# Kernel optimization log

Measured on AMD Instinct MI355X. Metric: run time of the kernel, lower is better.

## Reference

```python
import jax, jax.numpy as jnp
from jax import lax
import numpy as np

IMPOSSIBLE = -100000.0
B, S, T = 64, 2048, 128


def setup_inputs() -> dict:
    key = jax.random.key(0)
    k1, k2, k3, k4, k5, k6, k7 = jax.random.split(key, 7)
    emissions = jax.random.normal(k1, (B, S, T), dtype=jnp.float32)
    lengths = jax.random.randint(k2, (B,), S // 2, S + 1)  # ragged valid lengths
    mask = jnp.arange(S)[None, :] < lengths[:, None]       # (B,S) bool, contiguous
    tags = jax.random.randint(k3, (B, S), 0, T)
    forbidden_transitions = jax.random.bernoulli(k4, 0.3, (T, T))
    transitions = 0.1 * jax.random.normal(k5, (T, T), dtype=jnp.float32)
    start_transitions = 0.1 * jax.random.normal(k6, (T,), dtype=jnp.float32)
    end_transitions = 0.1 * jax.random.normal(k7, (T,), dtype=jnp.float32)
    return {
        'emissions': emissions,
        'mask': mask,
        'tags': tags,
        'forbidden_transitions': forbidden_transitions,
        'transitions': transitions,
        'start_transitions': start_transitions,
        'end_transitions': end_transitions,
    }


def _crf_nll(emissions, mask, tags, forbidden_transitions, transitions,
             start_transitions, end_transitions):
    # start/end forbidden default to all-False in the torch module, so only
    # pairwise transitions get masked.
    trans = jnp.where(forbidden_transitions, IMPOSSIBLE, transitions)  # (T,T)
    em = jnp.swapaxes(emissions, 0, 1)  # (S,B,T)
    m = mask.T                          # (S,B)
    tg = tags.T                         # (S,B)

    # ---- partition function z (logsumexp semiring forward scan) ----
    alpha0 = start_transitions[None, :] + em[0]  # (B,T)

    def fstep(alpha, xs):
        em_k, m_k = xs
        # res[b,j] = logsumexp_i( alpha[b,i] + trans[i,j] )
        res = jax.nn.logsumexp(alpha[:, :, None] + trans[None, :, :], axis=1)
        return jnp.where(m_k[:, None], res + em_k, alpha), None

    alphaF, _ = lax.scan(jax.checkpoint(fstep), alpha0, (em[1:], m[1:]))
    z = jax.nn.logsumexp(alphaF + end_transitions[None, :], axis=-1)  # (B,)

    # ---- posterior potential of the given tag sequence ----
    s0 = start_transitions[tg[0]] + jnp.take_along_axis(em[0], tg[0][:, None], axis=1)[:, 0]

    def pstep(s, xs):
        em_k, m_k, t_prev, t_k = xs
        sc = s + trans[t_prev, t_k] + jnp.take_along_axis(em_k, t_k[:, None], axis=1)[:, 0]
        return jnp.where(m_k, sc, s), None

    sF, _ = lax.scan(pstep, s0, (em[1:], m[1:], tg[:-1], tg[1:]))
    last_tag = jnp.take_along_axis(tags, (mask.sum(1) - 1)[:, None], axis=1)[:, 0]
    post = end_transitions[last_tag] + sF  # (B,)

    # torch shapes: posterior (1,B), z (1,B,1) -> broadcast (1,B,B); then mean.
    nll = post[None, None, :] - z[None, :, None]
    return jnp.mean(nll)


def reference(emissions, mask, tags, forbidden_transitions, transitions,
              start_transitions, end_transitions):
    return _crf_nll(emissions, mask, tags, forbidden_transitions, transitions,
                    start_transitions, end_transitions)
```

## Files before the change

kernel.cpp:

```cpp
#include <hip/hip_runtime.h>
#include <hip/hip_bf16.h>
#include <stdint.h>

#define BB 64
#define SS 2048
#define TT 128
#define GRP 6

typedef __bf16 bf16x8 __attribute__((ext_vector_type(8)));
typedef float  f32x4  __attribute__((ext_vector_type(4)));

__device__ __forceinline__ void wg_barrier_lds() {
    asm volatile("" ::: "memory");
    __builtin_amdgcn_s_waitcnt(0xc07f);
    __builtin_amdgcn_s_barrier();
    asm volatile("" ::: "memory");
}

__device__ __forceinline__ int detect_mode(const void* maskp) {
    uint32_t w0 = ((const uint32_t*)maskp)[0];
    if (w0 == 1u) return 0;
    if (w0 == 0x3F800000u) return 2;
    if (w0 == 0x3F803F80u) return 3;
    return 1;
}
__device__ __forceinline__ int mask_at(const void* maskp, int mode, size_t idx) {
    if (mode == 0) return ((const int*)maskp)[idx] != 0;
    if (mode == 1) return ((const unsigned char*)maskp)[idx] != 0;
    if (mode == 2) return ((const float*)maskp)[idx] != 0.f;
    return ((const unsigned short*)maskp)[idx] != 0;
}

__global__ __launch_bounds__(256, 1) void scan_kernel(
    const float* __restrict__ em, const void* __restrict__ maskp,
    const int* __restrict__ tags, const void* __restrict__ forb,
    const float* __restrict__ trans,
    const float* __restrict__ startt, const float* __restrict__ endt,
    double* __restrict__ CdW, float* __restrict__ pendW,
    float* __restrict__ uMW, double* __restrict__ postout)
{
    const int t = threadIdx.x;
    const int w = t >> 6;
    const int lane = t & 63;
    const int q = lane >> 4;
    const int c = lane & 15;
    const int bid = blockIdx.x;
    const bool isF = (bid < BB);
    const int b = isF ? bid : bid - BB;

    __shared__ __bf16 uS[2][TT];
    __shared__ __align__(16) float wred[4];
    __shared__ int    redi[4];
    __shared__ double redd[4];
    __shared__ int    redc[4];
    __shared__ float  Minit;

    const int mode = detect_mode(maskp);

    {
        int cnt = 0;
        for (int s = t; s < SS; s += 256) cnt += mask_at(maskp, mode, (size_t)b * SS + s);
        #pragma unroll
        for (int off = 32; off >= 1; off >>= 1) cnt += __shfl_xor(cnt, off);
        if (lane == 0) redi[w] = cnt;
    }
    __syncthreads();
    const int len = redi[0] + redi[1] + redi[2] + redi[3];

    const int mS    = len >> 1;
    const int steps = isF ? mS
                          : (len - 1 - mS);

    bf16x8 afrag[2][4];
    #pragma unroll
    for (int ml = 0; ml < 2; ++ml) {
        #pragma unroll
        for (int kt = 0; kt < 4; ++kt) {
            #pragma unroll
            for (int jj = 0; jj < 8; ++jj) {
                int row = isF ? (32 * kt + 8 * q + jj) : (32 * w + 16 * ml + c);
                int col = isF ? (32 * w + 16 * ml + c) : (32 * kt + 8 * q + jj);
                size_t idx = (size_t)row * TT + col;
                afrag[ml][kt][jj] = mask_at(forb, mode, idx) ? (__bf16)0.f
                                                             : (__bf16)__expf(trans[idx]);
            }
        }
    }

    const float* emB = em + (size_t)b * SS * TT;

    if (t < 16) {
        const float* base = isF ? startt : endt;
        const float* emI  = emB + (isF ? 0 : (size_t)(len - 1) * TT);
        float a[8]; float mx = -1e30f;
        #pragma unroll
        for (int jj = 0; jj < 8; ++jj) {
            int j = t * 8 + jj;
            a[jj] = base[j] + emI[j];
            mx = fmaxf(mx, a[jj]);
        }
        mx = fmaxf(mx, __shfl_xor(mx, 1)); mx = fmaxf(mx, __shfl_xor(mx, 2));
        mx = fmaxf(mx, __shfl_xor(mx, 4)); mx = fmaxf(mx, __shfl_xor(mx, 8));
        union { __bf16 h[8]; uint4 v; } pk;
        #pragma unroll
        for (int jj = 0; jj < 8; ++jj) pk.h[jj] = (__bf16)__expf(a[jj] - mx);
        *(uint4*)&uS[0][t * 8] = pk.v;
        if (t == 0) Minit = mx;
    }
    __syncthreads();

    double Cd = (double)Minit;
    float pending = 1.0f;

    const int tag0 = 32 * w + 4 * q;
    const int tag1 = tag0 + 16;

    int cur = 0;

    auto stepfn = [&](float4 e0, float4 e1, bool ren, bool scaleEm) {
        const __bf16* ub = &uS[cur][0];
        bf16x8 bf0 = *(const bf16x8*)(ub + 8 * q);
        bf16x8 bf1 = *(const bf16x8*)(ub + 32 + 8 * q);
        bf16x8 bf2 = *(const bf16x8*)(ub + 64 + 8 * q);
        bf16x8 bf3 = *(const bf16x8*)(ub + 96 + 8 * q);

        float sc00 = (scaleEm ? __expf(e0.x) : 1.0f) * pending;
        float sc01 = (scaleEm ? __expf(e0.y) : 1.0f) * pending;
        float sc02 = (scaleEm ? __expf(e0.z) : 1.0f) * pending;
        float sc03 = (scaleEm ? __expf(e0.w) : 1.0f) * pending;
        float sc10 = (scaleEm ? __expf(e1.x) : 1.0f) * pending;
        float sc11 = (scaleEm ? __expf(e1.y) : 1.0f) * pending;
        float sc12 = (scaleEm ? __expf(e1.z) : 1.0f) * pending;
        float sc13 = (scaleEm ? __expf(e1.w) : 1.0f) * pending;

        f32x4 aA0 = {0,0,0,0}, aB0 = {0,0,0,0}, aA1 = {0,0,0,0}, aB1 = {0,0,0,0};
        aA0 = __builtin_amdgcn_mfma_f32_16x16x32_bf16(afrag[0][0], bf0, aA0, 0, 0, 0);
        aA1 = __builtin_amdgcn_mfma_f32_16x16x32_bf16(afrag[1][0], bf0, aA1, 0, 0, 0);
        aB0 = __builtin_amdgcn_mfma_f32_16x16x32_bf16(afrag[0][2], bf2, aB0, 0, 0, 0);
        aB1 = __builtin_amdgcn_mfma_f32_16x16x32_bf16(afrag[1][2], bf2, aB1, 0, 0, 0);
        aA0 = __builtin_amdgcn_mfma_f32_16x16x32_bf16(afrag[0][1], bf1, aA0, 0, 0, 0);
        aA1 = __builtin_amdgcn_mfma_f32_16x16x32_bf16(afrag[1][1], bf1, aA1, 0, 0, 0);
        aB0 = __builtin_amdgcn_mfma_f32_16x16x32_bf16(afrag[0][3], bf3, aB0, 0, 0, 0);
        aB1 = __builtin_amdgcn_mfma_f32_16x16x32_bf16(afrag[1][3], bf3, aB1, 0, 0, 0);

        float v00 = (aA0[0] + aB0[0]) * sc00, v01 = (aA0[1] + aB0[1]) * sc01;
        float v02 = (aA0[2] + aB0[2]) * sc02, v03 = (aA0[3] + aB0[3]) * sc03;
        float v10 = (aA1[0] + aB1[0]) * sc10, v11 = (aA1[1] + aB1[1]) * sc11;
        float v12 = (aA1[2] + aB1[2]) * sc12, v13 = (aA1[3] + aB1[3]) * sc13;

        if (c == 0) {
            union { __bf16 h[4]; uint2 v; } p0, p1;
            p0.h[0] = (__bf16)v00; p0.h[1] = (__bf16)v01;
            p0.h[2] = (__bf16)v02; p0.h[3] = (__bf16)v03;
            p1.h[0] = (__bf16)v10; p1.h[1] = (__bf16)v11;
            p1.h[2] = (__bf16)v12; p1.h[3] = (__bf16)v13;
            __bf16* un = &uS[cur ^ 1][0];
            *(uint2*)(un + tag0) = p0.v;
            *(uint2*)(un + tag1) = p1.v;
        }
        if (ren) {
            float m = fmaxf(fmaxf(fmaxf(v00, v01), fmaxf(v02, v03)),
                            fmaxf(fmaxf(v10, v11), fmaxf(v12, v13)));
            m = fmaxf(m, __shfl_xor(m, 16));
            m = fmaxf(m, __shfl_xor(m, 32));
            if (lane == 0) wred[w] = m;
        }
        wg_barrier_lds();
        if (ren) {
            float4 wm = *(const float4*)wred;
            float M = fmaxf(fmaxf(wm.x, wm.y), fmaxf(wm.z, wm.w));
            pending = 1.0f / M;
            Cd += (double)__logf(M);
        } else {
            pending = 1.0f;
        }
        cur ^= 1;
    };

    int k = 0;
    float4 emc0[GRP], emc1[GRP];
    #pragma unroll
    for (int g = 0; g < GRP; ++g) {
        int kk = isF ? (1 + g) : (len - 2 - g);
        emc0[g] = *(const float4*)(emB + (size_t)kk * TT + tag0);
        emc1[g] = *(const float4*)(emB + (size_t)kk * TT + tag1);
    }

    while (k + GRP <= steps) {
        float4 emn0[GRP], emn1[GRP];
        #pragma unroll
        for (int g = 0; g < GRP; ++g) {
            int kk = isF ? (1 + k + GRP + g) : (len - 2 - (k + GRP + g));
            emn0[g] = *(const float4*)(emB + (size_t)kk * TT + tag0);
            emn1[g] = *(const float4*)(emB + (size_t)kk * TT + tag1);
        }
        #pragma unroll
        for (int g = 0; g < GRP; ++g)
            stepfn(emc0[g], emc1[g], g == GRP - 1, isF || (k + g != steps - 1));
        #pragma unroll
        for (int g = 0; g < GRP; ++g) { emc0[g] = emn0[g]; emc1[g] = emn1[g]; }
        k += GRP;
    }

    while (k < steps) {
        int kk = isF ? (1 + k) : (len - 2 - k);
        float4 e0 = *(const float4*)(emB + (size_t)kk * TT + tag0);
        float4 e1 = *(const float4*)(emB + (size_t)kk * TT + tag1);
        stepfn(e0, e1, true, isF || (k != steps - 1));
        ++k;
    }

    if (t < TT) uMW[(size_t)(isF ? 0 : BB) * TT + (size_t)b * TT + t] = (float)uS[cur][t];
    if (t == 0) { CdW[(isF ? 0 : BB) + b] = Cd; pendW[(isF ? 0 : BB) + b] = pending; }

    if (isF) {
        const int* tg = tags + (size_t)b * SS;
        double local = 0.0; int fcnt = 0;
        for (int kk = 1 + t; kk < len; kk += 256) {
            int tp = tg[kk - 1], tc = tg[kk];
            if (mask_at(forb, mode, (size_t)tp * TT + tc)) fcnt++;
            else local += (double)trans[tp * TT + tc];
            local += (double)emB[(size_t)kk * TT + tc];
        }
        if (t == 0) {
            local += (double)startt[tg[0]] + (double)emB[tg[0]];
            local += (double)endt[tg[len - 1]];
        }
        #pragma unroll
        for (int off = 32; off >= 1; off >>= 1) {
            local += __shfl_xor(local, off);
            fcnt  += __shfl_xor(fcnt, off);
        }
        if (lane == 0) { redd[w] = local; redc[w] = fcnt; }
        __syncthreads();
        if (t == 0) {
            double tot = redd[0] + redd[1] + redd[2] + redd[3];
            int fc = redc[0] + redc[1] + redc[2] + redc[3];
            postout[b] = tot - 100000.0 * (double)fc;
        }
    }
}

__global__ __launch_bounds__(1024) void fin_kernel(
    const double* __restrict__ CdW, const float* __restrict__ pendW,
    const float* __restrict__ uMW, const double* __restrict__ post,
    float* __restrict__ out)
{
    __shared__ double zS[BB];
    const int t = threadIdx.x, wv = t >> 6, lane = t & 63;
    for (int b = wv; b < BB; b += 16) {
        const float* uF = uMW + (size_t)b * TT;
        const float* uB = uMW + (size_t)(BB + b) * TT;
        float s = uF[lane] * uB[lane] + uF[lane + 64] * uB[lane + 64];
        #pragma unroll
        for (int off = 32; off >= 1; off >>= 1) s += __shfl_xor(s, off);
        if (lane == 0)
            zS[b] = CdW[b] + CdW[BB + b]
                  + log((double)pendW[b] * (double)pendW[BB + b] * (double)s);
    }
    __syncthreads();
    if (t < 64) {
        double pv = post[t];
        double zv = zS[t];
        #pragma unroll
        for (int off = 32; off >= 1; off >>= 1) {
            pv += __shfl_xor(pv, off);
            zv += __shfl_xor(zv, off);
        }
        if (t == 0) out[0] = (float)((pv - zv) / (double)BB);
    }
}

extern "C" void kernel_launch(void* const* d_in, const int* in_sizes, int n_in,
                              void* d_out, int out_size, void* d_ws, size_t ws_size,
                              hipStream_t stream) {
    const float* em     = (const float*)d_in[0];
    const void*  maskp  = d_in[1];
    const int*   tags   = (const int*)d_in[2];
    const void*  forb   = d_in[3];
    const float* trans  = (const float*)d_in[4];
    const float* startt = (const float*)d_in[5];
    const float* endt   = (const float*)d_in[6];

    double* post  = (double*)d_ws;
    double* CdW   = post + BB;
    float*  pendW = (float*)(CdW + 2 * BB);
    float*  uMW   = pendW + 2 * BB;

    scan_kernel<<<2 * BB, 256, 0, stream>>>(em, maskp, tags, forb, trans, startt, endt,
                                            CdW, pendW, uMW, post);
    fin_kernel<<<1, 1024, 0, stream>>>(CdW, pendW, uMW, post, (float*)d_out);
}
```

Measured before the change: 496.2 us.

## Split CRF forward scan into four segments using matrix-product middle chunks

Each sequence's scan is now cut into four parts instead of two. Forward and backward vector scans handle the ends, and two extra blocks per sequence compute full 128x128 transfer-matrix products over the middle segments, with swizzled LDS tiles. A new combine kernel applies the middle matrices to the end vectors and computes z in double precision. The serial dependency chain per block gets shorter at the price of about eight times more MFMA work per step in the middle blocks, twice as many workgroups at 512 threads, an extra kernel launch, and added bf16 rounding through the matrix products.

```diff
diff --git a/kernel.cpp b/kernel.cpp
--- a/kernel.cpp
+++ b/kernel.cpp
@@ -9,6 +9,8 @@
 
 typedef __bf16 bf16x8 __attribute__((ext_vector_type(8)));
 typedef float  f32x4  __attribute__((ext_vector_type(4)));
+
+#define SWZ(n) (((n) & 15) << 3)
 
 __device__ __forceinline__ void wg_barrier_lds() {
     asm volatile("" ::: "memory");
@@ -31,13 +33,27 @@
     return ((const unsigned short*)maskp)[idx] != 0;
 }
 
-__global__ __launch_bounds__(256, 1) void scan_kernel(
+struct EndSh {
+    __bf16 uS[2][TT];
+    float  wred[4];
+    int    redi[8];
+    double redd[8];
+    int    redc[8];
+    float  Minit;
+};
+struct MidSh {
+    __bf16 T[2][128][128];
+};
+union ShU { EndSh e; MidSh m; };
+
+__global__ __launch_bounds__(512) void scan_kernel(
     const float* __restrict__ em, const void* __restrict__ maskp,
     const int* __restrict__ tags, const void* __restrict__ forb,
     const float* __restrict__ trans,
     const float* __restrict__ startt, const float* __restrict__ endt,
     double* __restrict__ CdW, float* __restrict__ pendW,
-    float* __restrict__ uMW, double* __restrict__ postout)
+    float* __restrict__ uMW, double* __restrict__ lsW,
+    unsigned short* __restrict__ Tws, double* __restrict__ postout)
 {
     const int t = threadIdx.x;
     const int w = t >> 6;
@@ -45,230 +61,389 @@
     const int q = lane >> 4;
     const int c = lane & 15;
     const int bid = blockIdx.x;
+
+    __shared__ __align__(16) ShU sh;
+
+    const int mode = detect_mode(maskp);
+
+    const bool isEnd = (bid < 2 * BB);
     const bool isF = (bid < BB);
-    const int b = isF ? bid : bid - BB;
-
-    __shared__ __bf16 uS[2][TT];
-    __shared__ __align__(16) float wred[4];
-    __shared__ int    redi[4];
-    __shared__ double redd[4];
-    __shared__ int    redc[4];
-    __shared__ float  Minit;
-
-    const int mode = detect_mode(maskp);
+    const int seg = isEnd ? 0 : (bid - 2 * BB);
+    const int b = isEnd ? (isF ? bid : bid - BB) : (seg >> 1);
+    const int half = seg & 1;
 
     {
         int cnt = 0;
-        for (int s = t; s < SS; s += 256) cnt += mask_at(maskp, mode, (size_t)b * SS + s);
+        for (int s = t; s < SS; s += 512) cnt += mask_at(maskp, mode, (size_t)b * SS + s);
         #pragma unroll
         for (int off = 32; off >= 1; off >>= 1) cnt += __shfl_xor(cnt, off);
-        if (lane == 0) redi[w] = cnt;
+        if (lane == 0) sh.e.redi[w] = cnt;
     }
     __syncthreads();
-    const int len = redi[0] + redi[1] + redi[2] + redi[3];
-
-    const int mS    = len >> 1;
-    const int steps = isF ? mS
-                          : (len - 1 - mS);
-
-    bf16x8 afrag[2][4];
+    int len = 0;
     #pragma unroll
-    for (int ml = 0; ml < 2; ++ml) {
+    for (int i = 0; i < 8; ++i) len += sh.e.redi[i];
+    __syncthreads();
+
+    const int M  = ((len - 1) * 10) / 47;
+    const int E1 = ((len - 1) - 2 * M + 1) >> 1;
+    const int q1 = E1;
+    const int q2 = q1 + M;
+    const int q3 = q2 + M;
+    const int E2 = (len - 1) - q3;
+
+    const float* emB = em + (size_t)b * SS * TT;
+
+    if (isEnd) {
+        const int w4 = w & 3;
+        const int steps = isF ? q1 : E2;
+
+        bf16x8 afrag[2][4];
         #pragma unroll
-        for (int kt = 0; kt < 4; ++kt) {
+        for (int ml = 0; ml < 2; ++ml) {
+            #pragma unroll
+            for (int kt = 0; kt < 4; ++kt) {
+                #pragma unroll
+                for (int jj = 0; jj < 8; ++jj) {
+                    int row = isF ? (32 * kt + 8 * q + jj) : (32 * w4 + 16 * ml + c);
+                    int col = isF ? (32 * w4 + 16 * ml + c) : (32 * kt + 8 * q + jj);
+                    size_t idx = (size_t)row * TT + col;
+                    afrag[ml][kt][jj] = mask_at(forb, mode, idx) ? (__bf16)0.f
+                                                                 : (__bf16)__expf(trans[idx]);
+                }
+            }
+        }
+
+        if (t < 16) {
+            const float* base = isF ? startt : endt;
+            const float* emI  = emB + (isF ? 0 : (size_t)(len - 1) * TT);
+            float a[8]; float mx = -1e30f;
             #pragma unroll
             for (int jj = 0; jj < 8; ++jj) {
-                int row = isF ? (32 * kt + 8 * q + jj) : (32 * w + 16 * ml + c);
-                int col = isF ? (32 * w + 16 * ml + c) : (32 * kt + 8 * q + jj);
-                size_t idx = (size_t)row * TT + col;
-                afrag[ml][kt][jj] = mask_at(forb, mode, idx) ? (__bf16)0.f
-                                                             : (__bf16)__expf(trans[idx]);
-            }
-        }
-    }
-
-    const float* emB = em + (size_t)b * SS * TT;
-
-    if (t < 16) {
-        const float* base = isF ? startt : endt;
-        const float* emI  = emB + (isF ? 0 : (size_t)(len - 1) * TT);
-        float a[8]; float mx = -1e30f;
+                int j = t * 8 + jj;
+                a[jj] = base[j] + emI[j];
+                mx = fmaxf(mx, a[jj]);
+            }
+            mx = fmaxf(mx, __shfl_xor(mx, 1)); mx = fmaxf(mx, __shfl_xor(mx, 2));
+            mx = fmaxf(mx, __shfl_xor(mx, 4)); mx = fmaxf(mx, __shfl_xor(mx, 8));
+            union { __bf16 h[8]; uint4 v; } pk;
+            #pragma unroll
+            for (int jj = 0; jj < 8; ++jj) pk.h[jj] = (__bf16)__expf(a[jj] - mx);
+            *(uint4*)&sh.e.uS[0][t * 8] = pk.v;
+            if (t == 0) sh.e.Minit = mx;
+        }
+        __syncthreads();
+
+        double Cd = (double)sh.e.Minit;
+        float pending = 1.0f;
+        const int tag0 = 32 * w4 + 4 * q;
+        const int tag1 = tag0 + 16;
+        int cur = 0;
+
+        auto stepfn = [&](float4 e0, float4 e1, bool ren, bool scaleEm) {
+            const __bf16* ub = &sh.e.uS[cur][0];
+            bf16x8 bf0 = *(const bf16x8*)(ub + 8 * q);
+            bf16x8 bf1 = *(const bf16x8*)(ub + 32 + 8 * q);
+            bf16x8 bf2 = *(const bf16x8*)(ub + 64 + 8 * q);
+            bf16x8 bf3 = *(const bf16x8*)(ub + 96 + 8 * q);
+
+            float sc00 = (scaleEm ? __expf(e0.x) : 1.0f) * pending;
+            float sc01 = (scaleEm ? __expf(e0.y) : 1.0f) * pending;
+            float sc02 = (scaleEm ? __expf(e0.z) : 1.0f) * pending;
+            float sc03 = (scaleEm ? __expf(e0.w) : 1.0f) * pending;
+            float sc10 = (scaleEm ? __expf(e1.x) : 1.0f) * pending;
+            float sc11 = (scaleEm ? __expf(e1.y) : 1.0f) * pending;
+            float sc12 = (scaleEm ? __expf(e1.z) : 1.0f) * pending;
+            float sc13 = (scaleEm ? __expf(e1.w) : 1.0f) * pending;
+
+            f32x4 aA0 = {0,0,0,0}, aB0 = {0,0,0,0}, aA1 = {0,0,0,0}, aB1 = {0,0,0,0};
+            aA0 = __builtin_amdgcn_mfma_f32_16x16x32_bf16(afrag[0][0], bf0, aA0, 0, 0, 0);
+            aA1 = __builtin_amdgcn_mfma_f32_16x16x32_bf16(afrag[1][0], bf0, aA1, 0, 0, 0);
+            aB0 = __builtin_amdgcn_mfma_f32_16x16x32_bf16(afrag[0][2], bf2, aB0, 0, 0, 0);
+            aB1 = __builtin_amdgcn_mfma_f32_16x16x32_bf16(afrag[1][2], bf2, aB1, 0, 0, 0);
+            aA0 = __builtin_amdgcn_mfma_f32_16x16x32_bf16(afrag[0][1], bf1, aA0, 0, 0, 0);
+            aA1 = __builtin_amdgcn_mfma_f32_16x16x32_bf16(afrag[1][1], bf1, aA1, 0, 0, 0);
+            aB0 = __builtin_amdgcn_mfma_f32_16x16x32_bf16(afrag[0][3], bf3, aB0, 0, 0, 0);
+            aB1 = __builtin_amdgcn_mfma_f32_16x16x32_bf16(afrag[1][3], bf3, aB1, 0, 0, 0);
+
+            float v00 = (aA0[0] + aB0[0]) * sc00, v01 = (aA0[1] + aB0[1]) * sc01;
+            float v02 = (aA0[2] + aB0[2]) * sc02, v03 = (aA0[3] + aB0[3]) * sc03;
+            float v10 = (aA1[0] + aB1[0]) * sc10, v11 = (aA1[1] + aB1[1]) * sc11;
+            float v12 = (aA1[2] + aB1[2]) * sc12, v13 = (aA1[3] + aB1[3]) * sc13;
+
+            if (c == 0) {
+                union { __bf16 h[4]; uint2 v; } p0, p1;
+                p0.h[0] = (__bf16)v00; p0.h[1] = (__bf16)v01;
+                p0.h[2] = (__bf16)v02; p0.h[3] = (__bf16)v03;
+                p1.h[0] = (__bf16)v10; p1.h[1] = (__bf16)v11;
+                p1.h[2] = (__bf16)v12; p1.h[3] = (__bf16)v13;
+                __bf16* un = &sh.e.uS[cur ^ 1][0];
+                *(uint2*)(un + tag0) = p0.v;
+                *(uint2*)(un + tag1) = p1.v;
+            }
+            if (ren) {
+                float m = fmaxf(fmaxf(fmaxf(v00, v01), fmaxf(v02, v03)),
+                                fmaxf(fmaxf(v10, v11), fmaxf(v12, v13)));
+                m = fmaxf(m, __shfl_xor(m, 16));
+                m = fmaxf(m, __shfl_xor(m, 32));
+                if (lane == 0) sh.e.wred[w4] = m;
+            }
+            wg_barrier_lds();
+            if (ren) {
+                float4 wm = *(const float4*)sh.e.wred;
+                float Mx = fmaxf(fmaxf(wm.x, wm.y), fmaxf(wm.z, wm.w));
+                pending = 1.0f / Mx;
+                Cd += (double)__logf(Mx);
+            } else {
+                pending = 1.0f;
+            }
+            cur ^= 1;
+        };
+
+        int k = 0;
+        float4 emc0[GRP], emc1[GRP];
         #pragma unroll
-        for (int jj = 0; jj < 8; ++jj) {
-            int j = t * 8 + jj;
-            a[jj] = base[j] + emI[j];
-            mx = fmaxf(mx, a[jj]);
-        }
-        mx = fmaxf(mx, __shfl_xor(mx, 1)); mx = fmaxf(mx, __shfl_xor(mx, 2));
-        mx = fmaxf(mx, __shfl_xor(mx, 4)); mx = fmaxf(mx, __shfl_xor(mx, 8));
-        union { __bf16 h[8]; uint4 v; } pk;
+        for (int gg = 0; gg < GRP; ++gg) {
+            int g = isF ? gg : (GRP - 1 - gg);
+            int kk = isF ? (1 + g) : (len - 2 - g);
+            kk = kk < SS ? kk : SS - 1;
+            emc0[g] = *(const float4*)(emB + (size_t)kk * TT + tag0);
+            emc1[g] = *(const float4*)(emB + (size_t)kk * TT + tag1);
+        }
+
+        while (k + GRP <= steps) {
+            float4 emn0[GRP], emn1[GRP];
+            #pragma unroll
+            for (int gg = 0; gg < GRP; ++gg) {
+                int g = isF ? gg : (GRP - 1 - gg);
+                int kk = isF ? (1 + k + GRP + g) : (len - 2 - (k + GRP + g));
+                kk = kk < SS ? kk : SS - 1;
+                emn0[g] = *(const float4*)(emB + (size_t)kk * TT + tag0);
+                emn1[g] = *(const float4*)(emB + (size_t)kk * TT + tag1);
+            }
+            #pragma unroll
+            for (int g = 0; g < GRP; ++g)
+                stepfn(emc0[g], emc1[g], g == GRP - 1, isF || (k + g != steps - 1));
+            #pragma unroll
+            for (int g = 0; g < GRP; ++g) { emc0[g] = emn0[g]; emc1[g] = emn1[g]; }
+            k += GRP;
+        }
+        while (k < steps) {
+            int kk = isF ? (1 + k) : (len - 2 - k);
+            float4 e0 = *(const float4*)(emB + (size_t)kk * TT + tag0);
+            float4 e1 = *(const float4*)(emB + (size_t)kk * TT + tag1);
+            stepfn(e0, e1, true, isF || (k != steps - 1));
+            ++k;
+        }
+
+        __syncthreads();
+        if (t < TT) uMW[(size_t)(isF ? 0 : BB) * TT + (size_t)b * TT + t] = (float)sh.e.uS[cur][t];
+        if (t == 0) { CdW[(isF ? 0 : BB) + b] = Cd; pendW[(isF ? 0 : BB) + b] = pending; }
+
+        if (isF) {
+            const int* tg = tags + (size_t)b * SS;
+            double local = 0.0; int fcnt = 0;
+            for (int kk = 1 + t; kk < len; kk += 512) {
+                int tp = tg[kk - 1], tc = tg[kk];
+                if (mask_at(forb, mode, (size_t)tp * TT + tc)) fcnt++;
+                else local += (double)trans[tp * TT + tc];
+                local += (double)emB[(size_t)kk * TT + tc];
+            }
+            if (t == 0) {
+                local += (double)startt[tg[0]] + (double)emB[tg[0]];
+                local += (double)endt[tg[len - 1]];
+            }
+            #pragma unroll
+            for (int off = 32; off >= 1; off >>= 1) {
+                local += __shfl_xor(local, off);
+                fcnt  += __shfl_xor(fcnt, off);
+            }
+            if (lane == 0) { sh.e.redd[w] = local; sh.e.redc[w] = fcnt; }
+            __syncthreads();
+            if (t == 0) {
+                double tot = 0.0; int fc = 0;
+                #pragma unroll
+                for (int i = 0; i < 8; ++i) { tot += sh.e.redd[i]; fc += sh.e.redc[i]; }
+                postout[b] = tot - 100000.0 * (double)fc;
+            }
+        }
+    } else {
+        const int nc  = 16 * w + c;
+        const int swz = SWZ(nc);
+        const int ks  = half ? q2 : q1;
+        const int steps = M;
+
+        bf16x8 af[8][4];
         #pragma unroll
-        for (int jj = 0; jj < 8; ++jj) pk.h[jj] = (__bf16)__expf(a[jj] - mx);
-        *(uint4*)&uS[0][t * 8] = pk.v;
-        if (t == 0) Minit = mx;
+        for (int mt = 0; mt < 8; ++mt) {
+            #pragma unroll
+            for (int kt = 0; kt < 4; ++kt) {
+                #pragma unroll
+                for (int jj = 0; jj < 8; ++jj) {
+                    size_t idx = (size_t)(32 * kt + 8 * q + jj) * TT + (16 * mt + c);
+                    af[mt][kt][jj] = mask_at(forb, mode, idx) ? (__bf16)0.f
+                                                              : (__bf16)__expf(trans[idx]);
+                }
+            }
+        }
+
+        for (int p = t; p < 8192; p += 512) {
+            int n  = p >> 6;
+            int k2 = (p & 63) * 2;
+            unsigned int v = (k2 == n ? 0x3F80u : 0u) | (k2 + 1 == n ? 0x3F800000u : 0u);
+            *(unsigned int*)&sh.m.T[0][n][k2 ^ SWZ(n)] = v;
+        }
+        __syncthreads();
+
+        double Cdc = 0.0;
+        float pendc = 1.0f;
+        int cur = 0;
+
+        float4 emc[8];
+        #pragma unroll
+        for (int mt = 0; mt < 8; ++mt)
+            emc[mt] = *(const float4*)(emB + (size_t)(ks + 1) * TT + 16 * mt + 4 * q);
+
+        for (int s = 0; s < steps; ++s) {
+            const int k  = ks + 1 + s;
+            const int kn = (k + 1 < SS) ? (k + 1) : (SS - 1);
+            float4 emn[8];
+            #pragma unroll
+            for (int mt = 0; mt < 8; ++mt)
+                emn[mt] = *(const float4*)(emB + (size_t)kn * TT + 16 * mt + 4 * q);
+
+            bf16x8 bf[4];
+            #pragma unroll
+            for (int kt = 0; kt < 4; ++kt) {
+                int eo = (32 * kt + 8 * q) ^ swz;
+                bf[kt] = *(const bf16x8*)&sh.m.T[cur][nc][eo];
+            }
+
+            float sc[8][4];
+            #pragma unroll
+            for (int mt = 0; mt < 8; ++mt) {
+                sc[mt][0] = __expf(emc[mt].x) * pendc;
+                sc[mt][1] = __expf(emc[mt].y) * pendc;
+                sc[mt][2] = __expf(emc[mt].z) * pendc;
+                sc[mt][3] = __expf(emc[mt].w) * pendc;
+            }
+
+            f32x4 acc[8];
+            #pragma unroll
+            for (int mt = 0; mt < 8; ++mt) acc[mt] = (f32x4){0.f, 0.f, 0.f, 0.f};
+            #pragma unroll
+            for (int kt = 0; kt < 4; ++kt) {
+                #pragma unroll
+                for (int mt = 0; mt < 8; ++mt)
+                    acc[mt] = __builtin_amdgcn_mfma_f32_16x16x32_bf16(af[mt][kt], bf[kt], acc[mt], 0, 0, 0);
+            }
+
+            const bool ren = ((s % GRP) == GRP - 1) || (s == steps - 1);
+            float vm = 0.f;
+            #pragma unroll
+            for (int mt = 0; mt < 8; ++mt) {
+                float v0 = acc[mt][0] * sc[mt][0], v1 = acc[mt][1] * sc[mt][1];
+                float v2 = acc[mt][2] * sc[mt][2], v3 = acc[mt][3] * sc[mt][3];
+                vm = fmaxf(vm, fmaxf(fmaxf(v0, v1), fmaxf(v2, v3)));
+                union { __bf16 h[4]; uint2 u; } pk;
+                pk.h[0] = (__bf16)v0; pk.h[1] = (__bf16)v1;
+                pk.h[2] = (__bf16)v2; pk.h[3] = (__bf16)v3;
+                int eo = (16 * mt + 4 * q) ^ swz;
+                *(uint2*)&sh.m.T[cur ^ 1][nc][eo] = pk.u;
+            }
+            float Mc = 1.f;
+            if (ren) {
+                vm = fmaxf(vm, __shfl_xor(vm, 16));
+                vm = fmaxf(vm, __shfl_xor(vm, 32));
+                Mc = vm;
+            }
+            wg_barrier_lds();
+            if (ren) { pendc = 1.0f / Mc; Cdc += (double)__logf(Mc); }
+            else     { pendc = 1.0f; }
+            #pragma unroll
+            for (int mt = 0; mt < 8; ++mt) emc[mt] = emn[mt];
+            cur ^= 1;
+        }
+
+        __syncthreads();
+        if (lane < 16) lsW[(size_t)seg * 128 + 16 * w + lane] = Cdc + log((double)pendc);
+        for (int p = t; p < 8192; p += 512) {
+            int n  = p >> 6;
+            int k2 = (p & 63) * 2;
+            unsigned int v = *(const unsigned int*)&sh.m.T[cur][n][k2 ^ SWZ(n)];
+            *(unsigned int*)&Tws[(size_t)seg * 16384 + (size_t)n * 128 + k2] = v;
+        }
+    }
+}
+
+__global__ __launch_bounds__(128) void comb_kernel(
+    const double* __restrict__ CdW, const float* __restrict__ pendW,
+    const float* __restrict__ uMW, const double* __restrict__ lsW,
+    const unsigned short* __restrict__ Tws, double* __restrict__ zarr)
+{
+    const int b = blockIdx.x, i = threadIdx.x;
+    __shared__ double wv[128];
+    __shared__ double red[128];
+
+    double lsA = lsW[(size_t)(2 * b) * 128 + i];
+    float  xf  = uMW[(size_t)b * 128 + i];
+    double a1  = (xf > 0.f) ? lsA + log((double)xf) : -1e300;
+    red[i] = a1; __syncthreads();
+    for (int sdel = 64; sdel >= 1; sdel >>= 1) {
+        if (i < sdel) red[i] = fmax(red[i], red[i + sdel]);
+        __syncthreads();
+    }
+    double K1 = red[0]; __syncthreads();
+    wv[i] = (xf > 0.f) ? exp(a1 - K1) : 0.0; __syncthreads();
+
+    const unsigned short* TA = Tws + (size_t)(2 * b) * 16384;
+    double y = 0.0;
+    for (int n = 0; n < 128; ++n) {
+        unsigned int u = ((unsigned int)TA[(size_t)n * 128 + i]) << 16;
+        y += (double)__uint_as_float(u) * wv[n];
     }
     __syncthreads();
 
-    double Cd = (double)Minit;
-    float pending = 1.0f;
-
-    const int tag0 = 32 * w + 4 * q;
-    const int tag1 = tag0 + 16;
-
-    int cur = 0;
-
-    auto stepfn = [&](float4 e0, float4 e1, bool ren, bool scaleEm) {
-        const __bf16* ub = &uS[cur][0];
-        bf16x8 bf0 = *(const bf16x8*)(ub + 8 * q);
-        bf16x8 bf1 = *(const bf16x8*)(ub + 32 + 8 * q);
-        bf16x8 bf2 = *(const bf16x8*)(ub + 64 + 8 * q);
-        bf16x8 bf3 = *(const bf16x8*)(ub + 96 + 8 * q);
-
-        float sc00 = (scaleEm ? __expf(e0.x) : 1.0f) * pending;
-        float sc01 = (scaleEm ? __expf(e0.y) : 1.0f) * pending;
-        float sc02 = (scaleEm ? __expf(e0.z) : 1.0f) * pending;
-        float sc03 = (scaleEm ? __expf(e0.w) : 1.0f) * pending;
-        float sc10 = (scaleEm ? __expf(e1.x) : 1.0f) * pending;
-        float sc11 = (scaleEm ? __expf(e1.y) : 1.0f) * pending;
-        float sc12 = (scaleEm ? __expf(e1.z) : 1.0f) * pending;
-        float sc13 = (scaleEm ? __expf(e1.w) : 1.0f) * pending;
-
-        f32x4 aA0 = {0,0,0,0}, aB0 = {0,0,0,0}, aA1 = {0,0,0,0}, aB1 = {0,0,0,0};
-        aA0 = __builtin_amdgcn_mfma_f32_16x16x32_bf16(afrag[0][0], bf0, aA0, 0, 0, 0);
-        aA1 = __builtin_amdgcn_mfma_f32_16x16x32_bf16(afrag[1][0], bf0, aA1, 0, 0, 0);
-        aB0 = __builtin_amdgcn_mfma_f32_16x16x32_bf16(afrag[0][2], bf2, aB0, 0, 0, 0);
-        aB1 = __builtin_amdgcn_mfma_f32_16x16x32_bf16(afrag[1][2], bf2, aB1, 0, 0, 0);
-        aA0 = __builtin_amdgcn_mfma_f32_16x16x32_bf16(afrag[0][1], bf1, aA0, 0, 0, 0);
-        aA1 = __builtin_amdgcn_mfma_f32_16x16x32_bf16(afrag[1][1], bf1, aA1, 0, 0, 0);
-        aB0 = __builtin_amdgcn_mfma_f32_16x16x32_bf16(afrag[0][3], bf3, aB0, 0, 0, 0);
-        aB1 = __builtin_amdgcn_mfma_f32_16x16x32_bf16(afrag[1][3], bf3, aB1, 0, 0, 0);
-
-        float v00 = (aA0[0] + aB0[0]) * sc00, v01 = (aA0[1] + aB0[1]) * sc01;
-        float v02 = (aA0[2] + aB0[2]) * sc02, v03 = (aA0[3] + aB0[3]) * sc03;
-        float v10 = (aA1[0] + aB1[0]) * sc10, v11 = (aA1[1] + aB1[1]) * sc11;
-        float v12 = (aA1[2] + aB1[2]) * sc12, v13 = (aA1[3] + aB1[3]) * sc13;
-
-        if (c == 0) {
-            union { __bf16 h[4]; uint2 v; } p0, p1;
-            p0.h[0] = (__bf16)v00; p0.h[1] = (__bf16)v01;
-            p0.h[2] = (__bf16)v02; p0.h[3] = (__bf16)v03;
-            p1.h[0] = (__bf16)v10; p1.h[1] = (__bf16)v11;
-            p1.h[2] = (__bf16)v12; p1.h[3] = (__bf16)v13;
-            __bf16* un = &uS[cur ^ 1][0];
-            *(uint2*)(un + tag0) = p0.v;
-            *(uint2*)(un + tag1) = p1.v;
-        }
-        if (ren) {
-            float m = fmaxf(fmaxf(fmaxf(v00, v01), fmaxf(v02, v03)),
-                            fmaxf(fmaxf(v10, v11), fmaxf(v12, v13)));
-            m = fmaxf(m, __shfl_xor(m, 16));
-            m = fmaxf(m, __shfl_xor(m, 32));
-            if (lane == 0) wred[w] = m;
-        }
-        wg_barrier_lds();
-        if (ren) {
-            float4 wm = *(const float4*)wred;
-            float M = fmaxf(fmaxf(wm.x, wm.y), fmaxf(wm.z, wm.w));
-            pending = 1.0f / M;
-            Cd += (double)__logf(M);
-        } else {
-            pending = 1.0f;
-        }
-        cur ^= 1;
-    };
-
-    int k = 0;
-    float4 emc0[GRP], emc1[GRP];
+    double lsB = lsW[(size_t)(2 * b + 1) * 128 + i];
+    double a2  = (y > 0.0) ? lsB + log(y) : -1e300;
+    red[i] = a2; __syncthreads();
+    for (int sdel = 64; sdel >= 1; sdel >>= 1) {
+        if (i < sdel) red[i] = fmax(red[i], red[i + sdel]);
+        __syncthreads();
+    }
+    double K2 = red[0]; __syncthreads();
+    wv[i] = (y > 0.0) ? exp(a2 - K2) : 0.0; __syncthreads();
+
+    const unsigned short* TB = Tws + (size_t)(2 * b + 1) * 16384;
+    double s = 0.0;
+    for (int n = 0; n < 128; ++n) {
+        unsigned int u = ((unsigned int)TB[(size_t)n * 128 + i]) << 16;
+        s += (double)__uint_as_float(u) * wv[n];
+    }
+    double g = (double)uMW[(size_t)(BB + b) * 128 + i];
+    red[i] = s * g; __syncthreads();
+    for (int sdel = 64; sdel >= 1; sdel >>= 1) {
+        if (i < sdel) red[i] += red[i + sdel];
+        __syncthreads();
+    }
+    if (i == 0) {
+        zarr[b] = CdW[b] + log((double)pendW[b])
+                + CdW[BB + b] + log((double)pendW[BB + b])
+                + K1 + K2 + log(red[0]);
+    }
+}
+
+__global__ void fin_kernel(const double* __restrict__ z, const double* __restrict__ post,
+                           float* __restrict__ out) {
+    int t = threadIdx.x;
+    double pv = post[t];
+    double zv = z[t];
     #pragma unroll
-    for (int g = 0; g < GRP; ++g) {
-        int kk = isF ? (1 + g) : (len - 2 - g);
-        emc0[g] = *(const float4*)(emB + (size_t)kk * TT + tag0);
-        emc1[g] = *(const float4*)(emB + (size_t)kk * TT + tag1);
-    }
-
-    while (k + GRP <= steps) {
-        float4 emn0[GRP], emn1[GRP];
-        #pragma unroll
-        for (int g = 0; g < GRP; ++g) {
-            int kk = isF ? (1 + k + GRP + g) : (len - 2 - (k + GRP + g));
-            emn0[g] = *(const float4*)(emB + (size_t)kk * TT + tag0);
-            emn1[g] = *(const float4*)(emB + (size_t)kk * TT + tag1);
-        }
-        #pragma unroll
-        for (int g = 0; g < GRP; ++g)
-            stepfn(emc0[g], emc1[g], g == GRP - 1, isF || (k + g != steps - 1));
-        #pragma unroll
-        for (int g = 0; g < GRP; ++g) { emc0[g] = emn0[g]; emc1[g] = emn1[g]; }
-        k += GRP;
-    }
-
-    while (k < steps) {
-        int kk = isF ? (1 + k) : (len - 2 - k);
-        float4 e0 = *(const float4*)(emB + (size_t)kk * TT + tag0);
-        float4 e1 = *(const float4*)(emB + (size_t)kk * TT + tag1);
-        stepfn(e0, e1, true, isF || (k != steps - 1));
-        ++k;
-    }
-
-    if (t < TT) uMW[(size_t)(isF ? 0 : BB) * TT + (size_t)b * TT + t] = (float)uS[cur][t];
-    if (t == 0) { CdW[(isF ? 0 : BB) + b] = Cd; pendW[(isF ? 0 : BB) + b] = pending; }
-
-    if (isF) {
-        const int* tg = tags + (size_t)b * SS;
-        double local = 0.0; int fcnt = 0;
-        for (int kk = 1 + t; kk < len; kk += 256) {
-            int tp = tg[kk - 1], tc = tg[kk];
-            if (mask_at(forb, mode, (size_t)tp * TT + tc)) fcnt++;
-            else local += (double)trans[tp * TT + tc];
-            local += (double)emB[(size_t)kk * TT + tc];
-        }
-        if (t == 0) {
-            local += (double)startt[tg[0]] + (double)emB[tg[0]];
-            local += (double)endt[tg[len - 1]];
-        }
-        #pragma unroll
-        for (int off = 32; off >= 1; off >>= 1) {
-            local += __shfl_xor(local, off);
-            fcnt  += __shfl_xor(fcnt, off);
-        }
-        if (lane == 0) { redd[w] = local; redc[w] = fcnt; }
-        __syncthreads();
-        if (t == 0) {
-            double tot = redd[0] + redd[1] + redd[2] + redd[3];
-            int fc = redc[0] + redc[1] + redc[2] + redc[3];
-            postout[b] = tot - 100000.0 * (double)fc;
-        }
-    }
-}
-
-__global__ __launch_bounds__(1024) void fin_kernel(
-    const double* __restrict__ CdW, const float* __restrict__ pendW,
-    const float* __restrict__ uMW, const double* __restrict__ post,
-    float* __restrict__ out)
-{
-    __shared__ double zS[BB];
-    const int t = threadIdx.x, wv = t >> 6, lane = t & 63;
-    for (int b = wv; b < BB; b += 16) {
-        const float* uF = uMW + (size_t)b * TT;
-        const float* uB = uMW + (size_t)(BB + b) * TT;
-        float s = uF[lane] * uB[lane] + uF[lane + 64] * uB[lane + 64];
-        #pragma unroll
-        for (int off = 32; off >= 1; off >>= 1) s += __shfl_xor(s, off);
-        if (lane == 0)
-            zS[b] = CdW[b] + CdW[BB + b]
-                  + log((double)pendW[b] * (double)pendW[BB + b] * (double)s);
-    }
-    __syncthreads();
-    if (t < 64) {
-        double pv = post[t];
-        double zv = zS[t];
-        #pragma unroll
-        for (int off = 32; off >= 1; off >>= 1) {
-            pv += __shfl_xor(pv, off);
-            zv += __shfl_xor(zv, off);
-        }
-        if (t == 0) out[0] = (float)((pv - zv) / (double)BB);
-    }
+    for (int off = 32; off >= 1; off >>= 1) {
+        pv += __shfl_xor(pv, off);
+        zv += __shfl_xor(zv, off);
+    }
+    if (t == 0) out[0] = (float)((pv - zv) / (double)BB);
 }
 
 extern "C" void kernel_launch(void* const* d_in, const int* in_sizes, int n_in,
@@ -283,11 +458,15 @@
     const float* endt   = (const float*)d_in[6];
 
     double* post  = (double*)d_ws;
-    double* CdW   = post + BB;
-    float*  pendW = (float*)(CdW + 2 * BB);
+    double* zarr  = post + BB;
+    double* CdW   = zarr + BB;
+    double* lsW   = CdW + 2 * BB;
+    float*  pendW = (float*)(lsW + 128 * 128);
     float*  uMW   = pendW + 2 * BB;
-
-    scan_kernel<<<2 * BB, 256, 0, stream>>>(em, maskp, tags, forb, trans, startt, endt,
-                                            CdW, pendW, uMW, post);
-    fin_kernel<<<1, 1024, 0, stream>>>(CdW, pendW, uMW, post, (float*)d_out);
-}
+    unsigned short* Tws = (unsigned short*)(uMW + 128 * 128);
+
+    scan_kernel<<<4 * BB, 512, 0, stream>>>(em, maskp, tags, forb, trans, startt, endt,
+                                            CdW, pendW, uMW, lsW, Tws, post);
+    comb_kernel<<<BB, 128, 0, stream>>>(CdW, pendW, uMW, lsW, Tws, zarr);
+    fin_kernel<<<1, 64, 0, stream>>>(zarr, post, (float*)d_out);
+}
```

Result: slower. 1.319 ms (+165.8%).
